# Kernel optimization log

Measured on AMD Instinct MI355X. Metric: run time of the kernel, lower is better.

## Reference

```python
import jax, jax.numpy as jnp
import numpy as np

N = 262144        # examples
N_RULES = 128     # weak labeling functions
D_L = 128         # extra feature dim of x_l
NHIDDEN = 256
NCLASS = 10
NFEAT = N_RULES + D_L


def setup_inputs() -> dict:
    key = jax.random.key(0)
    k1, k2, k3, k4 = jax.random.split(key, 4)
    # weak-rule votes: -1 = abstain, 0..NCLASS-1 = class vote (stored as float, as in torch)
    x_lf = jax.random.randint(k1, (N, N_RULES), -1, NCLASS).astype(jnp.float32)
    x_l = jax.random.normal(k2, (N, D_L), dtype=jnp.float32)
    W1 = jax.random.normal(k3, (NFEAT, NHIDDEN), dtype=jnp.float32) / np.sqrt(NFEAT).astype(np.float32)
    b1 = jnp.zeros((NHIDDEN,), jnp.float32)
    W2 = jax.random.normal(k4, (NHIDDEN, N_RULES), dtype=jnp.float32) / np.sqrt(NHIDDEN).astype(np.float32)
    b2 = jnp.zeros((N_RULES,), jnp.float32)
    return {"x_lf": x_lf, "x_l": x_l, "W1": W1, "b1": b1, "W2": W2, "b2": b2}


def reference(x_lf, x_l, W1, b1, W2, b2):
    # MLP attention scores over rules
    x = jnp.concatenate([x_lf, x_l], axis=1)            # (N, NFEAT)
    z = jnp.tanh(x @ W1 + b1) @ W2 + b2                 # (N, N_RULES)
    score = jax.nn.softmax(z, axis=1)                   # (N, N_RULES)
    mask = (x_lf >= 0).astype(score.dtype)
    coverage_score = score * mask                       # (N, N_RULES)
    # bucket-sum of scores by voted class (single-pass scatter-add instead of
    # the original O(nclass) masked-reduction loop); abstains (-1) -> bucket NCLASS, dropped
    idx = jnp.where(x_lf >= 0, x_lf.astype(jnp.int32), NCLASS)  # (N, N_RULES)
    score_matrix = jax.vmap(
        lambda s, i: jax.ops.segment_sum(s, i, num_segments=NCLASS + 1)
    )(score, idx)[:, :NCLASS]                           # (N, NCLASS)
    softmax_new_y = jax.nn.log_softmax(score_matrix, axis=1)
    return softmax_new_y, coverage_score
```

## Files before the change

kernel.cpp:

```cpp
#include <hip/hip_runtime.h>
#include <hip/hip_bf16.h>

#define NRULES 128
#define NH 256
#define NC 10
#define NF 256
#define BM 128

typedef __attribute__((ext_vector_type(8))) __bf16 bf16x8;
typedef __attribute__((ext_vector_type(4))) float f32x4;
typedef __attribute__((ext_vector_type(4))) int i32x4;

static __device__ __forceinline__ unsigned int f2bf_bits(float f) {
    unsigned int u = __float_as_uint(f);
    u += 0x7fffu + ((u >> 16) & 1u);
    return u >> 16;
}

static __device__ __forceinline__ float tanh_fast(float x) {
    float xc = fminf(fmaxf(x, -15.f), 15.f);
    float e = __expf(2.f * xc);
    return 1.f - 2.f * __builtin_amdgcn_rcpf(e + 1.f);
}

__global__ __launch_bounds__(256) void prep_transpose(
    const float* __restrict__ W1, const float* __restrict__ W2,
    unsigned short* __restrict__ W1T, unsigned short* __restrict__ W2T)
{
    __shared__ float tile[64][65];
    const int b = blockIdx.x;
    const float* src;
    unsigned short* dst;
    int sstride;
    if (b < 16) {
        int ti = b >> 2, tj = b & 3;
        src = W1 + ti * 64 * 256 + tj * 64;  sstride = 256;
        dst = W1T + tj * 64 * 256 + ti * 64;
    } else {
        int bb = b - 16;
        int ti = bb >> 1, tj = bb & 1;
        src = W2 + ti * 64 * 128 + tj * 64;  sstride = 128;
        dst = W2T + tj * 64 * 256 + ti * 64;
    }
    const int t = threadIdx.x;
    #pragma unroll
    for (int i = 0; i < 4; ++i) {
        int idx = i * 256 + t;
        int r = idx >> 4, c4 = (idx & 15) * 4;
        f32x4 v = *(const f32x4*)(src + r * sstride + c4);
        tile[r][c4 + 0] = v.x; tile[r][c4 + 1] = v.y;
        tile[r][c4 + 2] = v.z; tile[r][c4 + 3] = v.w;
    }
    __syncthreads();
    #pragma unroll
    for (int i = 0; i < 2; ++i) {
        int idx = i * 256 + t;
        int rr = idx >> 3, cc = (idx & 7) * 8;
        i32x4 pk;
        #pragma unroll
        for (int j = 0; j < 4; ++j) {
            unsigned int lo = f2bf_bits(tile[cc + 2 * j][rr]);
            unsigned int hi = f2bf_bits(tile[cc + 2 * j + 1][rr]);
            pk[j] = (int)(lo | (hi << 16));
        }
        *(i32x4*)(dst + rr * 256 + cc) = pk;
    }
}

__global__ __launch_bounds__(256, 2) void fused_mlp_attn(
    const float* __restrict__ x_lf, const float* __restrict__ x_l,
    const float* __restrict__ b1, const float* __restrict__ b2,
    const unsigned short* __restrict__ W1T, const unsigned short* __restrict__ W2T,
    float* __restrict__ out0, float* __restrict__ out1)
{
    __shared__ __align__(16) unsigned char smem[BM * 512 + BM * 68];
    unsigned char* Xs = smem;
    unsigned char* Vs = smem + BM * 512;

    const int tid = threadIdx.x;
    const long e0 = (long)blockIdx.x * BM;

    #pragma unroll
    for (int i = 0; i < 16; ++i) {
        int idx = i * 256 + tid;
        int e = idx >> 5;
        int c = idx & 31;
        const float* src = (c < 16) ? (x_lf + (e0 + e) * 128 + c * 8)
                                    : (x_l  + (e0 + e) * 128 + (c - 16) * 8);
        f32x4 a  = *(const f32x4*)src;
        f32x4 bq = *(const f32x4*)(src + 4);
        i32x4 pk;
        pk[0] = (int)(f2bf_bits(a.x)  | (f2bf_bits(a.y)  << 16));
        pk[1] = (int)(f2bf_bits(a.z)  | (f2bf_bits(a.w)  << 16));
        pk[2] = (int)(f2bf_bits(bq.x) | (f2bf_bits(bq.y) << 16));
        pk[3] = (int)(f2bf_bits(bq.z) | (f2bf_bits(bq.w) << 16));
        *(i32x4*)(Xs + e * 512 + ((c ^ (e & 7)) << 4)) = pk;
        if (c < 16) {
            unsigned int v = 0;
            v |= (unsigned int)((int)a.x  + 1);
            v |= (unsigned int)((int)a.y  + 1) << 4;
            v |= (unsigned int)((int)a.z  + 1) << 8;
            v |= (unsigned int)((int)a.w  + 1) << 12;
            v |= (unsigned int)((int)bq.x + 1) << 16;
            v |= (unsigned int)((int)bq.y + 1) << 20;
            v |= (unsigned int)((int)bq.z + 1) << 24;
            v |= (unsigned int)((int)bq.w + 1) << 28;
            *(unsigned int*)(Vs + e * 68 + c * 4) = v;
        }
    }
    __syncthreads();

    const int wv  = tid >> 6;
    const int lane = tid & 63;
    const int q   = lane >> 4;
    const int l15 = lane & 15;

    const int hb = wv * 64;
    f32x4 acc[4][8];
    #pragma unroll
    for (int mt = 0; mt < 4; ++mt)
        #pragma unroll
        for (int nt = 0; nt < 8; ++nt)
            acc[mt][nt] = (f32x4){0.f, 0.f, 0.f, 0.f};

    for (int kk = 0; kk < 8; ++kk) {
        const int k = kk * 32 + q * 8;
        bf16x8 af[4];
        #pragma unroll
        for (int mt = 0; mt < 4; ++mt)
            af[mt] = *(const bf16x8*)(W1T + (hb + mt * 16 + l15) * 256 + k);
        const int cc = kk * 4 + q;
        bf16x8 bfq[8];
        #pragma unroll
        for (int nt = 0; nt < 8; ++nt) {
            int e = nt * 16 + l15;
            bfq[nt] = *(const bf16x8*)(Xs + e * 512 + ((cc ^ (e & 7)) << 4));
        }
        #pragma unroll
        for (int mt = 0; mt < 4; ++mt)
            #pragma unroll
            for (int nt = 0; nt < 8; ++nt)
                acc[mt][nt] = __builtin_amdgcn_mfma_f32_16x16x32_bf16(
                    af[mt], bfq[nt], acc[mt][nt], 0, 0, 0);
    }

    #pragma unroll
    for (int mt = 0; mt < 4; ++mt) {
        f32x4 bv = *(const f32x4*)(b1 + hb + mt * 16 + q * 4);
        #pragma unroll
        for (int nt = 0; nt < 8; ++nt)
            #pragma unroll
            for (int j = 0; j < 4; ++j)
                acc[mt][nt][j] = tanh_fast(acc[mt][nt][j] + bv[j]);
    }

    __syncthreads();

    #pragma unroll
    for (int mt = 0; mt < 4; ++mt) {
        int h = hb + mt * 16 + q * 4;
        int c16 = h >> 3;
        int sub = (h & 4) << 1;
        #pragma unroll
        for (int nt = 0; nt < 8; ++nt) {
            int e = nt * 16 + l15;
            uint2 d;
            d.x = f2bf_bits(acc[mt][nt][0]) | (f2bf_bits(acc[mt][nt][1]) << 16);
            d.y = f2bf_bits(acc[mt][nt][2]) | (f2bf_bits(acc[mt][nt][3]) << 16);
            *(uint2*)(Xs + e * 512 + ((c16 ^ (e & 7)) << 4) + sub) = d;
        }
    }
    __syncthreads();

    const int eb = wv * 32;
    f32x4 acc2[8][2];
    #pragma unroll
    for (int mt = 0; mt < 8; ++mt)
        #pragma unroll
        for (int nt = 0; nt < 2; ++nt)
            acc2[mt][nt] = (f32x4){0.f, 0.f, 0.f, 0.f};

    for (int kk = 0; kk < 8; ++kk) {
        const int k = kk * 32 + q * 8;
        bf16x8 af2[8];
        #pragma unroll
        for (int mt = 0; mt < 8; ++mt)
            af2[mt] = *(const bf16x8*)(W2T + (mt * 16 + l15) * 256 + k);
        const int cc = kk * 4 + q;
        bf16x8 bf2[2];
        #pragma unroll
        for (int nt = 0; nt < 2; ++nt) {
            int e = eb + nt * 16 + l15;
            bf2[nt] = *(const bf16x8*)(Xs + e * 512 + ((cc ^ (e & 7)) << 4));
        }
        #pragma unroll
        for (int mt = 0; mt < 8; ++mt)
            #pragma unroll
            for (int nt = 0; nt < 2; ++nt)
                acc2[mt][nt] = __builtin_amdgcn_mfma_f32_16x16x32_bf16(
                    af2[mt], bf2[nt], acc2[mt][nt], 0, 0, 0);
    }

    #pragma unroll
    for (int nt = 0; nt < 2; ++nt) {
        const int e = eb + nt * 16 + l15;

        #pragma unroll
        for (int mt = 0; mt < 8; ++mt) {
            f32x4 bv = *(const f32x4*)(b2 + mt * 16 + q * 4);
            acc2[mt][nt] += bv;
        }

        int vt[8];
        #pragma unroll
        for (int mt = 0; mt < 8; ++mt)
            vt[mt] = *(const unsigned short*)(Vs + e * 68 + mt * 8 + q * 2);

        float m = -3.4e38f;
        #pragma unroll
        for (int mt = 0; mt < 8; ++mt)
            #pragma unroll
            for (int j = 0; j < 4; ++j)
                m = fmaxf(m, acc2[mt][nt][j]);
        m = fmaxf(m, __shfl_xor(m, 16));
        m = fmaxf(m, __shfl_xor(m, 32));

        float s = 0.f;
        #pragma unroll
        for (int mt = 0; mt < 8; ++mt)
            #pragma unroll
            for (int j = 0; j < 4; ++j) {
                float p = __expf(acc2[mt][nt][j] - m);
                acc2[mt][nt][j] = p;
                s += p;
            }
        s += __shfl_xor(s, 16);
        s += __shfl_xor(s, 32);
        const float inv = __builtin_amdgcn_rcpf(s);

        float bucket[NC];
        #pragma unroll
        for (int c = 0; c < NC; ++c) bucket[c] = 0.f;

        #pragma unroll
        for (int mt = 0; mt < 8; ++mt) {
            int u = vt[mt];
            f32x4 cov;
            #pragma unroll
            for (int j = 0; j < 4; ++j) {
                float sc = acc2[mt][nt][j] * inv;
                int v = (u >> (4 * j)) & 15;
                cov[j] = (v != 0) ? sc : 0.f;
                #pragma unroll
                for (int c = 0; c < NC; ++c)
                    bucket[c] += (v == c + 1) ? sc : 0.f;
            }
            *(f32x4*)(out1 + (e0 + e) * 128 + mt * 16 + q * 4) = cov;
        }

        #pragma unroll
        for (int c = 0; c < NC; ++c) {
            bucket[c] += __shfl_xor(bucket[c], 16);
            bucket[c] += __shfl_xor(bucket[c], 32);
        }

        float m10 = bucket[0];
        #pragma unroll
        for (int c = 1; c < NC; ++c) m10 = fmaxf(m10, bucket[c]);
        float se = 0.f;
        #pragma unroll
        for (int c = 0; c < NC; ++c) se += __expf(bucket[c] - m10);
        const float lse = m10 + __logf(se);

        if (q == 0) {
            float* o = out0 + (e0 + e) * 10;
            #pragma unroll
            for (int c = 0; c < NC; ++c) o[c] = bucket[c] - lse;
        }
    }
}

extern "C" void kernel_launch(void* const* d_in, const int* in_sizes, int n_in,
                              void* d_out, int out_size, void* d_ws, size_t ws_size,
                              hipStream_t stream)
{
    const float* x_lf = (const float*)d_in[0];
    const float* x_l  = (const float*)d_in[1];
    const float* W1   = (const float*)d_in[2];
    const float* b1   = (const float*)d_in[3];
    const float* W2   = (const float*)d_in[4];
    const float* b2   = (const float*)d_in[5];
    const int n = in_sizes[0] / NRULES;
    float* out0 = (float*)d_out;
    float* out1 = out0 + (long)n * NC;
    unsigned short* W1T = (unsigned short*)d_ws;
    unsigned short* W2T = W1T + NH * NF;

    prep_transpose<<<24, 256, 0, stream>>>(W1, W2, W1T, W2T);
    fused_mlp_attn<<<n / BM, 256, 0, stream>>>(x_lf, x_l, b1, b2, W1T, W2T,
                                               out0, out1);
}
```

Baseline: 444.9 us.

## Use 512-thread blocks with eight waves splitting hidden and example tiles

Doubles the block size to 8 waves. Each wave now computes 32 hidden units in the first GEMM and 16 examples in the second GEMM and softmax epilogue, which cuts per-wave accumulator registers and raises occupancy (launch bounds 512,4). Manual bf16 bit packing is replaced with native __bf16 conversions. The trade-off is that more waves now reload the W1/W2 fragments from global memory, and the larger blocks synchronise more threads at each barrier.

```diff
diff --git a/kernel.cpp b/kernel.cpp
--- a/kernel.cpp
+++ b/kernel.cpp
@@ -8,6 +8,7 @@
 #define BM 128
 
 typedef __attribute__((ext_vector_type(8))) __bf16 bf16x8;
+typedef __attribute__((ext_vector_type(4))) __bf16 bf16x4;
 typedef __attribute__((ext_vector_type(4))) float f32x4;
 typedef __attribute__((ext_vector_type(4))) int i32x4;
 
@@ -67,7 +68,7 @@
     }
 }
 
-__global__ __launch_bounds__(256, 2) void fused_mlp_attn(
+__global__ __launch_bounds__(512, 4) void fused_mlp_attn(
     const float* __restrict__ x_lf, const float* __restrict__ x_l,
     const float* __restrict__ b1, const float* __restrict__ b2,
     const unsigned short* __restrict__ W1T, const unsigned short* __restrict__ W2T,
@@ -81,20 +82,20 @@
     const long e0 = (long)blockIdx.x * BM;
 
     #pragma unroll
-    for (int i = 0; i < 16; ++i) {
-        int idx = i * 256 + tid;
+    for (int i = 0; i < 8; ++i) {
+        int idx = i * 512 + tid;
         int e = idx >> 5;
         int c = idx & 31;
         const float* src = (c < 16) ? (x_lf + (e0 + e) * 128 + c * 8)
                                     : (x_l  + (e0 + e) * 128 + (c - 16) * 8);
         f32x4 a  = *(const f32x4*)src;
         f32x4 bq = *(const f32x4*)(src + 4);
-        i32x4 pk;
-        pk[0] = (int)(f2bf_bits(a.x)  | (f2bf_bits(a.y)  << 16));
-        pk[1] = (int)(f2bf_bits(a.z)  | (f2bf_bits(a.w)  << 16));
-        pk[2] = (int)(f2bf_bits(bq.x) | (f2bf_bits(bq.y) << 16));
-        pk[3] = (int)(f2bf_bits(bq.z) | (f2bf_bits(bq.w) << 16));
-        *(i32x4*)(Xs + e * 512 + ((c ^ (e & 7)) << 4)) = pk;
+        bf16x8 pk;
+        pk[0] = (__bf16)a.x;  pk[1] = (__bf16)a.y;
+        pk[2] = (__bf16)a.z;  pk[3] = (__bf16)a.w;
+        pk[4] = (__bf16)bq.x; pk[5] = (__bf16)bq.y;
+        pk[6] = (__bf16)bq.z; pk[7] = (__bf16)bq.w;
+        *(bf16x8*)(Xs + e * 512 + ((c ^ (e & 7)) << 4)) = pk;
         if (c < 16) {
             unsigned int v = 0;
             v |= (unsigned int)((int)a.x  + 1);
@@ -115,19 +116,19 @@
     const int q   = lane >> 4;
     const int l15 = lane & 15;
 
-    const int hb = wv * 64;
-    f32x4 acc[4][8];
-    #pragma unroll
-    for (int mt = 0; mt < 4; ++mt)
+    const int hb = wv * 32;
+    f32x4 acc[2][8];
+    #pragma unroll
+    for (int mt = 0; mt < 2; ++mt)
         #pragma unroll
         for (int nt = 0; nt < 8; ++nt)
             acc[mt][nt] = (f32x4){0.f, 0.f, 0.f, 0.f};
 
     for (int kk = 0; kk < 8; ++kk) {
         const int k = kk * 32 + q * 8;
-        bf16x8 af[4];
-        #pragma unroll
-        for (int mt = 0; mt < 4; ++mt)
+        bf16x8 af[2];
+        #pragma unroll
+        for (int mt = 0; mt < 2; ++mt)
             af[mt] = *(const bf16x8*)(W1T + (hb + mt * 16 + l15) * 256 + k);
         const int cc = kk * 4 + q;
         bf16x8 bfq[8];
@@ -137,7 +138,7 @@
             bfq[nt] = *(const bf16x8*)(Xs + e * 512 + ((cc ^ (e & 7)) << 4));
         }
         #pragma unroll
-        for (int mt = 0; mt < 4; ++mt)
+        for (int mt = 0; mt < 2; ++mt)
             #pragma unroll
             for (int nt = 0; nt < 8; ++nt)
                 acc[mt][nt] = __builtin_amdgcn_mfma_f32_16x16x32_bf16(
@@ -145,7 +146,7 @@
     }
 
     #pragma unroll
-    for (int mt = 0; mt < 4; ++mt) {
+    for (int mt = 0; mt < 2; ++mt) {
         f32x4 bv = *(const f32x4*)(b1 + hb + mt * 16 + q * 4);
         #pragma unroll
         for (int nt = 0; nt < 8; ++nt)
@@ -157,28 +158,26 @@
     __syncthreads();
 
     #pragma unroll
-    for (int mt = 0; mt < 4; ++mt) {
+    for (int mt = 0; mt < 2; ++mt) {
         int h = hb + mt * 16 + q * 4;
         int c16 = h >> 3;
         int sub = (h & 4) << 1;
         #pragma unroll
         for (int nt = 0; nt < 8; ++nt) {
             int e = nt * 16 + l15;
-            uint2 d;
-            d.x = f2bf_bits(acc[mt][nt][0]) | (f2bf_bits(acc[mt][nt][1]) << 16);
-            d.y = f2bf_bits(acc[mt][nt][2]) | (f2bf_bits(acc[mt][nt][3]) << 16);
-            *(uint2*)(Xs + e * 512 + ((c16 ^ (e & 7)) << 4) + sub) = d;
-        }
-    }
-    __syncthreads();
-
-    const int eb = wv * 32;
-    f32x4 acc2[8][2];
+            bf16x4 d;
+            d[0] = (__bf16)acc[mt][nt][0]; d[1] = (__bf16)acc[mt][nt][1];
+            d[2] = (__bf16)acc[mt][nt][2]; d[3] = (__bf16)acc[mt][nt][3];
+            *(bf16x4*)(Xs + e * 512 + ((c16 ^ (e & 7)) << 4) + sub) = d;
+        }
+    }
+    __syncthreads();
+
+    const int eb = wv * 16;
+    f32x4 acc2[8];
     #pragma unroll
     for (int mt = 0; mt < 8; ++mt)
-        #pragma unroll
-        for (int nt = 0; nt < 2; ++nt)
-            acc2[mt][nt] = (f32x4){0.f, 0.f, 0.f, 0.f};
+        acc2[mt] = (f32x4){0.f, 0.f, 0.f, 0.f};
 
     for (int kk = 0; kk < 8; ++kk) {
         const int k = kk * 32 + q * 8;
@@ -187,28 +186,21 @@
         for (int mt = 0; mt < 8; ++mt)
             af2[mt] = *(const bf16x8*)(W2T + (mt * 16 + l15) * 256 + k);
         const int cc = kk * 4 + q;
-        bf16x8 bf2[2];
-        #pragma unroll
-        for (int nt = 0; nt < 2; ++nt) {
-            int e = eb + nt * 16 + l15;
-            bf2[nt] = *(const bf16x8*)(Xs + e * 512 + ((cc ^ (e & 7)) << 4));
-        }
-        #pragma unroll
-        for (int mt = 0; mt < 8; ++mt)
-            #pragma unroll
-            for (int nt = 0; nt < 2; ++nt)
-                acc2[mt][nt] = __builtin_amdgcn_mfma_f32_16x16x32_bf16(
-                    af2[mt], bf2[nt], acc2[mt][nt], 0, 0, 0);
-    }
-
-    #pragma unroll
-    for (int nt = 0; nt < 2; ++nt) {
-        const int e = eb + nt * 16 + l15;
+        int e = eb + l15;
+        bf16x8 bf2 = *(const bf16x8*)(Xs + e * 512 + ((cc ^ (e & 7)) << 4));
+        #pragma unroll
+        for (int mt = 0; mt < 8; ++mt)
+            acc2[mt] = __builtin_amdgcn_mfma_f32_16x16x32_bf16(
+                af2[mt], bf2, acc2[mt], 0, 0, 0);
+    }
+
+    {
+        const int e = eb + l15;
 
         #pragma unroll
         for (int mt = 0; mt < 8; ++mt) {
             f32x4 bv = *(const f32x4*)(b2 + mt * 16 + q * 4);
-            acc2[mt][nt] += bv;
+            acc2[mt] += bv;
         }
 
         int vt[8];
@@ -221,7 +213,7 @@
         for (int mt = 0; mt < 8; ++mt)
             #pragma unroll
             for (int j = 0; j < 4; ++j)
-                m = fmaxf(m, acc2[mt][nt][j]);
+                m = fmaxf(m, acc2[mt][j]);
         m = fmaxf(m, __shfl_xor(m, 16));
         m = fmaxf(m, __shfl_xor(m, 32));
 
@@ -230,8 +222,8 @@
         for (int mt = 0; mt < 8; ++mt)
             #pragma unroll
             for (int j = 0; j < 4; ++j) {
-                float p = __expf(acc2[mt][nt][j] - m);
-                acc2[mt][nt][j] = p;
+                float p = __expf(acc2[mt][j] - m);
+                acc2[mt][j] = p;
                 s += p;
             }
         s += __shfl_xor(s, 16);
@@ -248,7 +240,7 @@
             f32x4 cov;
             #pragma unroll
             for (int j = 0; j < 4; ++j) {
-                float sc = acc2[mt][nt][j] * inv;
+                float sc = acc2[mt][j] * inv;
                 int v = (u >> (4 * j)) & 15;
                 cov[j] = (v != 0) ? sc : 0.f;
                 #pragma unroll
@@ -297,6 +289,6 @@
     unsigned short* W2T = W1T + NH * NF;
 
     prep_transpose<<<24, 256, 0, stream>>>(W1, W2, W1T, W2T);
-    fused_mlp_attn<<<n / BM, 256, 0, stream>>>(x_lf, x_l, b1, b2, W1T, W2T,
+    fused_mlp_attn<<<n / BM, 512, 0, stream>>>(x_lf, x_l, b1, b2, W1T, W2T,
                                                out0, out1);
 }
```

New measurement: 479.0 us. 7.7% more time.

## Replace register bucket reduction with LDS atomics and reload votes from global

Applied to the files above, without the earlier changes.

Per-class bucket sums are no longer accumulated with a 10-way compare-select per score and then shuffle-reduced. Each live score is now atomically added into a per-example LDS bucket array, and a final pass over 128 threads computes log-softmax and writes out0. The packed 4-bit vote table in LDS is removed, and votes are re-read from x_lf in global memory. Float-to-bf16 conversion now uses native casts instead of manual rounding, and the tanh clamp is dropped. The LDS atomics may contend because all four quad lanes of an example hit the same 10 buckets, and the extra global reads of x_lf add memory traffic.

```diff
diff --git a/kernel.cpp b/kernel.cpp
--- a/kernel.cpp
+++ b/kernel.cpp
@@ -8,6 +8,7 @@
 #define BM 128
 
 typedef __attribute__((ext_vector_type(8))) __bf16 bf16x8;
+typedef __attribute__((ext_vector_type(4))) __bf16 bf16x4;
 typedef __attribute__((ext_vector_type(4))) float f32x4;
 typedef __attribute__((ext_vector_type(4))) int i32x4;
 
@@ -18,8 +19,7 @@
 }
 
 static __device__ __forceinline__ float tanh_fast(float x) {
-    float xc = fminf(fmaxf(x, -15.f), 15.f);
-    float e = __expf(2.f * xc);
+    float e = __expf(2.f * x);
     return 1.f - 2.f * __builtin_amdgcn_rcpf(e + 1.f);
 }
 
@@ -73,12 +73,16 @@
     const unsigned short* __restrict__ W1T, const unsigned short* __restrict__ W2T,
     float* __restrict__ out0, float* __restrict__ out1)
 {
-    __shared__ __align__(16) unsigned char smem[BM * 512 + BM * 68];
+    __shared__ __align__(16) unsigned char smem[BM * 512 + BM * 10 * 4];
     unsigned char* Xs = smem;
-    unsigned char* Vs = smem + BM * 512;
+    float* lbuck = (float*)(smem + BM * 512);
 
     const int tid = threadIdx.x;
     const long e0 = (long)blockIdx.x * BM;
+
+    #pragma unroll
+    for (int i = 0; i < 5; ++i)
+        lbuck[i * 256 + tid] = 0.f;
 
     #pragma unroll
     for (int i = 0; i < 16; ++i) {
@@ -89,24 +93,12 @@
                                     : (x_l  + (e0 + e) * 128 + (c - 16) * 8);
         f32x4 a  = *(const f32x4*)src;
         f32x4 bq = *(const f32x4*)(src + 4);
-        i32x4 pk;
-        pk[0] = (int)(f2bf_bits(a.x)  | (f2bf_bits(a.y)  << 16));
-        pk[1] = (int)(f2bf_bits(a.z)  | (f2bf_bits(a.w)  << 16));
-        pk[2] = (int)(f2bf_bits(bq.x) | (f2bf_bits(bq.y) << 16));
-        pk[3] = (int)(f2bf_bits(bq.z) | (f2bf_bits(bq.w) << 16));
-        *(i32x4*)(Xs + e * 512 + ((c ^ (e & 7)) << 4)) = pk;
-        if (c < 16) {
-            unsigned int v = 0;
-            v |= (unsigned int)((int)a.x  + 1);
-            v |= (unsigned int)((int)a.y  + 1) << 4;
-            v |= (unsigned int)((int)a.z  + 1) << 8;
-            v |= (unsigned int)((int)a.w  + 1) << 12;
-            v |= (unsigned int)((int)bq.x + 1) << 16;
-            v |= (unsigned int)((int)bq.y + 1) << 20;
-            v |= (unsigned int)((int)bq.z + 1) << 24;
-            v |= (unsigned int)((int)bq.w + 1) << 28;
-            *(unsigned int*)(Vs + e * 68 + c * 4) = v;
-        }
+        bf16x8 pk;
+        pk[0] = (__bf16)a.x;  pk[1] = (__bf16)a.y;
+        pk[2] = (__bf16)a.z;  pk[3] = (__bf16)a.w;
+        pk[4] = (__bf16)bq.x; pk[5] = (__bf16)bq.y;
+        pk[6] = (__bf16)bq.z; pk[7] = (__bf16)bq.w;
+        *(bf16x8*)(Xs + e * 512 + ((c ^ (e & 7)) << 4)) = pk;
     }
     __syncthreads();
 
@@ -164,10 +156,10 @@
         #pragma unroll
         for (int nt = 0; nt < 8; ++nt) {
             int e = nt * 16 + l15;
-            uint2 d;
-            d.x = f2bf_bits(acc[mt][nt][0]) | (f2bf_bits(acc[mt][nt][1]) << 16);
-            d.y = f2bf_bits(acc[mt][nt][2]) | (f2bf_bits(acc[mt][nt][3]) << 16);
-            *(uint2*)(Xs + e * 512 + ((c16 ^ (e & 7)) << 4) + sub) = d;
+            bf16x4 d;
+            d[0] = (__bf16)acc[mt][nt][0]; d[1] = (__bf16)acc[mt][nt][1];
+            d[2] = (__bf16)acc[mt][nt][2]; d[3] = (__bf16)acc[mt][nt][3];
+            *(bf16x4*)(Xs + e * 512 + ((c16 ^ (e & 7)) << 4) + sub) = d;
         }
     }
     __syncthreads();
@@ -211,10 +203,10 @@
             acc2[mt][nt] += bv;
         }
 
-        int vt[8];
-        #pragma unroll
-        for (int mt = 0; mt < 8; ++mt)
-            vt[mt] = *(const unsigned short*)(Vs + e * 68 + mt * 8 + q * 2);
+        f32x4 vr[8];
+        #pragma unroll
+        for (int mt = 0; mt < 8; ++mt)
+            vr[mt] = *(const f32x4*)(x_lf + (e0 + e) * 128 + mt * 16 + q * 4);
 
         float m = -3.4e38f;
         #pragma unroll
@@ -238,45 +230,37 @@
         s += __shfl_xor(s, 32);
         const float inv = __builtin_amdgcn_rcpf(s);
 
-        float bucket[NC];
-        #pragma unroll
-        for (int c = 0; c < NC; ++c) bucket[c] = 0.f;
-
+        float* lb = lbuck + e * 10;
         #pragma unroll
         for (int mt = 0; mt < 8; ++mt) {
-            int u = vt[mt];
             f32x4 cov;
             #pragma unroll
             for (int j = 0; j < 4; ++j) {
                 float sc = acc2[mt][nt][j] * inv;
-                int v = (u >> (4 * j)) & 15;
-                cov[j] = (v != 0) ? sc : 0.f;
-                #pragma unroll
-                for (int c = 0; c < NC; ++c)
-                    bucket[c] += (v == c + 1) ? sc : 0.f;
+                float v = vr[mt][j];
+                bool live = (v >= 0.f);
+                cov[j] = live ? sc : 0.f;
+                if (live) atomicAdd(lb + (int)v, sc);
             }
             *(f32x4*)(out1 + (e0 + e) * 128 + mt * 16 + q * 4) = cov;
         }
-
-        #pragma unroll
-        for (int c = 0; c < NC; ++c) {
-            bucket[c] += __shfl_xor(bucket[c], 16);
-            bucket[c] += __shfl_xor(bucket[c], 32);
-        }
-
-        float m10 = bucket[0];
-        #pragma unroll
-        for (int c = 1; c < NC; ++c) m10 = fmaxf(m10, bucket[c]);
+    }
+    __syncthreads();
+
+    if (tid < BM) {
+        float b[NC];
+        #pragma unroll
+        for (int c = 0; c < NC; ++c) b[c] = lbuck[tid * 10 + c];
+        float m10 = b[0];
+        #pragma unroll
+        for (int c = 1; c < NC; ++c) m10 = fmaxf(m10, b[c]);
         float se = 0.f;
         #pragma unroll
-        for (int c = 0; c < NC; ++c) se += __expf(bucket[c] - m10);
+        for (int c = 0; c < NC; ++c) se += __expf(b[c] - m10);
         const float lse = m10 + __logf(se);
-
-        if (q == 0) {
-            float* o = out0 + (e0 + e) * 10;
-            #pragma unroll
-            for (int c = 0; c < NC; ++c) o[c] = bucket[c] - lse;
-        }
+        float* o = out0 + (e0 + tid) * 10;
+        #pragma unroll
+        for (int c = 0; c < NC; ++c) o[c] = b[c] - lse;
     }
 }
 
```

Result: slower. 516.4 us (+16.1%).
